# Optimization experiments

Hardware: AMD Instinct MI355X
Metric: run time of the kernel (lower is better)

The kernel has to match this reference:

```python
import jax, jax.numpy as jnp
import numpy as np

B, T, NB = 8, 120, 40
VD, WD = 2053, 300
H, E, NH, HD = 512, 256, 8, 64
SEG, NSEG = 12, 10
IDX = np.round(np.linspace(SEG - 1, T - 1, NSEG)).astype(int)  # segment endpoints


def setup_inputs():
    keys = iter(jax.random.split(jax.random.key(0), 64))
    def w(*shape):
        return jax.random.normal(next(keys), shape, jnp.float32) * 0.02
    z = lambda *s: jnp.zeros(s, jnp.float32)
    return dict(
        videos=jax.random.normal(next(keys), (B, T, NB, VD), jnp.float32),
        sub_glove=jax.random.normal(next(keys), (B, WD), jnp.float32),
        obj_glove=jax.random.normal(next(keys), (B, WD), jnp.float32),
        W_ev=w(VD - 5, E), b_ev=z(E),
        W_el=w(5, E), b_el=z(E),
        W_ew=w(WD, E), b_ew=z(E),
        W_sp1=w(2 * E, E), b_sp1=z(E), w_sp2=w(E),
        W_s2o=w(NB, E), b_s2o=z(E),
        W_o2s=w(NB, E), b_o2s=z(E),
        W_tv=w(H, H), b_tv=z(H),
        Wq=w(H, H), bq=z(H), Wk=w(H, H), bk=z(H), Wv=w(H, H), bv=z(H), Wo=w(H, H), bo=z(H),
        g1=jnp.ones(H, jnp.float32), be1=z(H),
        Wf1=w(H, H), bf1=z(H), Wf2=w(H, H), bf2=z(H),
        g2=jnp.ones(H, jnp.float32), be2=z(H),
        W_tr=w(H, H), b_tr=z(H),
        W_tb1=w(2 * H, H), b_tb1=z(H), w_tb2=w(H),
        W_ih=w(4 * H, H), W_hh=w(4 * H, H), b_ih=z(4 * H), b_hh=z(4 * H),
        W_l1=w(2 * H, H), b_l1=z(H), w_l2=w(H),
    )


def reference(videos, sub_glove, obj_glove, W_ev, b_ev, W_el, b_el, W_ew, b_ew,
              W_sp1, b_sp1, w_sp2, W_s2o, b_s2o, W_o2s, b_o2s, W_tv, b_tv,
              Wq, bq, Wk, bk, Wv, bv, Wo, bo, g1, be1, Wf1, bf1, Wf2, bf2, g2, be2,
              W_tr, b_tr, W_tb1, b_tb1, w_tb2, W_ih, W_hh, b_ih, b_hh, W_l1, b_l1, w_l2):
    relu = jax.nn.relu
    # spatialAtt (vectorized over batch; dropout = identity, eval mode)
    ve = relu(videos[..., :VD - 5] @ W_ev + b_ev) + relu(videos[..., VD - 5:] @ W_el + b_el)  # [B,T,NB,E]
    sub_e = relu(sub_glove @ W_ew + b_ew)  # [B,E]
    obj_e = relu(obj_glove @ W_ew + b_ew)

    def attend(word):  # additive attention over bboxes per frame
        wb = jnp.broadcast_to(word[:, None, None, :], ve.shape)
        s = jnp.tanh(jnp.concatenate([ve, wb], -1) @ W_sp1 + b_sp1) @ w_sp2  # [B,T,NB]
        a = jax.nn.softmax(s, -1)
        return jnp.einsum('btn,btne->bte', a, ve), a

    sub_feat, sub_att = attend(sub_e)
    obj_feat, obj_att = attend(obj_e)
    s2o = relu(sub_att @ W_s2o + b_s2o)  # msg_sub2obj on attention weights [B,T,NB]->[B,T,E]
    o2s = relu(obj_att @ W_o2s + b_o2s)
    ori_x = jnp.concatenate([sub_feat + o2s, obj_feat + s2o], -1)  # [B,T,H]
    rel = jnp.concatenate([sub_e, obj_e], -1)[:, None, :]  # [B,1,H]

    def ln(zz, g, b):
        m = zz.mean(-1, keepdims=True)
        v = jnp.mean((zz - m) ** 2, -1, keepdims=True)
        return (zz - m) * jax.lax.rsqrt(v + 1e-5) * g + b

    # transform_visual + 1-layer post-norm TransformerEncoder (relu FFN, dropout=identity)
    x = relu(ori_x @ W_tv + b_tv)
    q = (x @ Wq + bq).reshape(B, T, NH, HD)
    k = (x @ Wk + bk).reshape(B, T, NH, HD)
    v = (x @ Wv + bv).reshape(B, T, NH, HD)
    att = jax.nn.softmax(jnp.einsum('bqhd,bkhd->bhqk', q, k) / np.float32(np.sqrt(HD)), -1)
    ao = jnp.einsum('bhqk,bkhd->bqhd', att, v).reshape(B, T, H) @ Wo + bo
    x = ln(x + ao, g1, be1)
    x = ln(x + relu(x @ Wf1 + bf1) @ Wf2 + bf2, g2, be2)
    within = x  # [B,T,H]

    seg_in = within[:, IDX, :]  # [B,NSEG,H]
    tr = relu(rel @ W_tr + b_tr)
    ctx = jnp.broadcast_to(tr, seg_in.shape)
    beta2 = jax.nn.softmax(jnp.tanh(jnp.concatenate([seg_in, ctx], -1) @ W_tb1 + b_tb1) @ w_tb2, -1)  # [B,NSEG]

    # torch-convention LSTM (gates i,f,g,o); note attention weights are NOT applied to input (vfeat=input)
    def step(carry, xt):
        h, c = carry
        gates = xt @ W_ih.T + h @ W_hh.T + b_ih + b_hh
        i, f, g_, o = jnp.split(gates, 4, -1)
        c = jax.nn.sigmoid(f) * c + jax.nn.sigmoid(i) * jnp.tanh(g_)
        h = jax.nn.sigmoid(o) * jnp.tanh(c)
        return (h, c), h

    (hT, cT), _ = jax.lax.scan(step, (jnp.zeros((B, H), within.dtype), jnp.zeros((B, H), within.dtype)),
                               seg_in.transpose(1, 0, 2))

    ctx2 = jnp.broadcast_to(hT[:, None, :], within.shape)
    beta1 = jax.nn.softmax(jnp.tanh(jnp.concatenate([within, ctx2], -1) @ W_l1 + b_l1) @ w_l2, -1)  # [B,T]
    temp = beta1 + jnp.repeat(beta2, SEG, axis=1)  # temp[:,i] = beta1[:,i] + beta2[:,i//12]
    output = jnp.einsum('bt,bth->bh', temp, within)  # [B,H]
    return output, hT, cT, sub_att, obj_att, beta1, beta2
```

## Files before the change

### kernel.cpp

```cpp
#include <hip/hip_runtime.h>
#include <cstddef>
#include <cstdint>

#define B_ 8
#define T_ 120
#define NB_ 40
#define VD_ 2053
#define E_ 256
#define H_ 512
#define M_ 38400
#define R_ 960

static constexpr size_t OFF_VE    = 0;
static constexpr size_t OFF_SSUB  = OFF_VE + (size_t)M_ * E_;
static constexpr size_t OFF_SOBJ  = OFF_SSUB + M_;
static constexpr size_t OFF_WBS   = OFF_SOBJ + M_;
static constexpr size_t OFF_WBO   = OFF_WBS + B_ * E_;
static constexpr size_t OFF_TBIAS = OFF_WBO + B_ * E_;
static constexpr size_t OFF_ORIX  = OFF_TBIAS + B_ * H_;
static constexpr size_t OFF_X     = OFF_ORIX + (size_t)R_ * H_;
static constexpr size_t OFF_Q     = OFF_X    + (size_t)R_ * H_;
static constexpr size_t OFF_K     = OFF_Q    + (size_t)R_ * H_;
static constexpr size_t OFF_V     = OFF_K    + (size_t)R_ * H_;
static constexpr size_t OFF_AO    = OFF_V    + (size_t)R_ * H_;
// ... 156 lines not shown
      t[r][c] = src[(size_t)(kb * 64 + r) * 512 + nb * 64 + c];
    }
    __syncthreads();
#pragma unroll
    for (int i = 0; i < 16; ++i) {
      int idx = tid + 256 * i; int n = idx >> 6, kk = idx & 63;
      dst[(size_t)(nb * 64 + n) * 512 + kb * 64 + kk] = f2bf(t[kk][n]);
    }
  } else if (bid < 592) {
    int b2 = bid - 576;
    int kb = b2 >> 2, nb = b2 & 3;
#pragma unroll
    for (int i = 0; i < 16; ++i) {
      int idx = tid + 256 * i; int r = idx >> 6, c = idx & 63;
      t[r][c] = W_sp1[(size_t)(kb * 64 + r) * 256 + nb * 64 + c];
    }
    __syncthreads();
#pragma unroll
    for (int i = 0; i < 16; ++i) {
      int idx = tid + 256 * i; int n = idx >> 6, kk = idx & 63;
      wsp1bf[(size_t)(nb * 64 + n) * 256 + kb * 64 + kk] = f2bf(t[kk][n]);
    }
  } else if (bid < 656) {
    int b2 = bid - 592;
    int kb = b2 >> 3, nb = b2 & 7;
#pragma unroll
    for (int i = 0; i < 16; ++i) {
      int idx = tid + 256 * i; int r = idx >> 6, c = idx & 63;
      t[r][c] = W_l1[(size_t)(kb * 64 + r) * 512 + nb * 64 + c];
    }
    __syncthreads();
#pragma unroll
    for (int i = 0; i < 16; ++i) {
      int idx = tid + 256 * i; int n = idx >> 6, kk = idx & 63;
      wl1bf[(size_t)(nb * 64 + n) * 512 + kb * 64 + kk] = f2bf(t[kk][n]);
    }
  } else if (bid < 1680) {
    int i = (bid - 656) * 256 + tid;
    const float* s; unsigned short* d; int off;
    if (i < 131072) { s = W_ih; d = wihbf; off = i * 8; }
    else            { s = W_hh; d = whhbf; off = (i - 131072) * 8; }
    float f[8];
#pragma unroll
    for (int j = 0; j < 8; ++j) f[j] = s[off + j];
    *(short8*)(d + off) = mk8(f);
  } else if (bid == 1680) {
    for (int i = tid; i < 12288; i += 256) hz[i] = 0.f;
  } else {
    int b = bid - 1681;
    float* sg = shm;
    float* og = shm + 300;
    float* se = shm + 600;
    float* oe = shm + 856;
    float* trl = shm + 1112;
    for (int i = tid; i < 300; i += 256) { sg[i] = sub_g[b * 300 + i]; og[i] = obj_g[b * 300 + i]; }
    __syncthreads();
    {
      float a1 = b_ew[tid], a2 = a1;
      for (int w = 0; w < 300; ++w) {
        float we = W_ew[w * 256 + tid];
        a1 += sg[w] * we; a2 += og[w] * we;
      }
      se[tid] = fmaxf(a1, 0.f); oe[tid] = fmaxf(a2, 0.f);
    }
    __syncthreads();
    {
      float a1 = b_sp1[tid], a2 = a1;
      for (int e = 0; e < 256; ++e) {
        float ww = W_sp1[(256 + e) * 256 + tid];
        a1 += se[e] * ww; a2 += oe[e] * ww;
      }
      wbs[b * 256 + tid] = a1; wbo[b * 256 + tid] = a2;
    }
    for (int jj = 0; jj < 2; ++jj) {
      int j = tid + jj * 256;
      float a = b_tr[j];
      for (int i = 0; i < 256; ++i) a += se[i] * W_tr[i * 512 + j];
      for (int i = 0; i < 256; ++i) a += oe[i] * W_tr[(256 + i) * 512 + j];
      trl[j] = fmaxf(a, 0.f);
    }
    __syncthreads();
    for (int jj = 0; jj < 2; ++jj) {
      int j = tid + jj * 256;
      float a = b_tb1[j];
      for (int i = 0; i < 512; ++i) a += trl[i] * W_tb1[(size_t)(512 + i) * 512 + j];
      tbias[b * 512 + j] = a;
    }
  }
}

__global__ __launch_bounds__(256) void k_wconvT(const float* __restrict__ src,
                                                unsigned short* __restrict__ dst,
                                                int K, int N) {
  __shared__ float t[64][65];
  int nblk = N >> 6;
  int kb = blockIdx.x / nblk, nb = blockIdx.x - kb * nblk;
  int tid = threadIdx.x;
#pragma unroll
  for (int i = 0; i < 16; ++i) {
    int idx = tid + 256 * i;
    int r = idx >> 6, c = idx & 63;
    t[r][c] = src[(size_t)(kb * 64 + r) * N + nb * 64 + c];
  }
  __syncthreads();
#pragma unroll
  for (int i = 0; i < 16; ++i) {
    int idx = tid + 256 * i;
    int n = idx >> 6, kk = idx & 63;
    dst[(size_t)(nb * 64 + n) * K + kb * 64 + kk] = f2bf(t[kk][n]);
  }
}

__global__ __launch_bounds__(256) void k_wconv7(
    const float* __restrict__ w0, const float* __restrict__ w1,
    const float* __restrict__ w2, const float* __restrict__ w3,
    const float* __restrict__ w4, const float* __restrict__ w5,
    const float* __restrict__ w6, unsigned short* __restrict__ dstb) {
  __shared__ float t[64][65];
  int wsel = blockIdx.x >> 6, sub = blockIdx.x & 63;
  int kb = sub >> 3, nb = sub & 7;
  const float* src = wsel == 0 ? w0 : wsel == 1 ? w1 : wsel == 2 ? w2
                   : wsel == 3 ? w3 : wsel == 4 ? w4 : wsel == 5 ? w5 : w6;
  unsigned short* dst = dstb + (size_t)wsel * 262144;
  int tid = threadIdx.x;
#pragma unroll
  for (int i = 0; i < 16; ++i) {
    int idx = tid + 256 * i;
    int r = idx >> 6, c = idx & 63;
    t[r][c] = src[(size_t)(kb * 64 + r) * 512 + nb * 64 + c];
  }
  __syncthreads();
#pragma unroll
  for (int i = 0; i < 16; ++i) {
    int idx = tid + 256 * i;
    int n = idx >> 6, kk = idx & 63;
    dst[(size_t)(nb * 64 + n) * 512 + kb * 64 + kk] = f2bf(t[kk][n]);
  }
}

__global__ __launch_bounds__(256) void k_cvt2(const float* __restrict__ a,
                                              const float* __restrict__ b,
                                              unsigned short* __restrict__ da,
                                              unsigned short* __restrict__ db) {
  int i = blockIdx.x * 256 + threadIdx.x;
  const float* s; unsigned short* d; int off;
  if (i < 131072) { s = a; d = da; off = i * 8; }
  else            { s = b; d = db; off = (i - 131072) * 8; }
  float f[8];
#pragma unroll
  for (int j = 0; j < 8; ++j) f[j] = s[off + j];
  *(short8*)(d + off) = mk8(f);
}

__global__ __launch_bounds__(512) void k_gemm_ve_m97(
    const float* __restrict__ videos, const unsigned short* __restrict__ wtbf,
    const float* __restrict__ bev, const float* __restrict__ Wel,
    const float* __restrict__ bel, unsigned short* __restrict__ vebf) {
  __shared__ __align__(16) unsigned short lds[20480];
  int tid = threadIdx.x;
  int rowbase = blockIdx.x * 64;
  int lane = tid & 63, wid = tid >> 6;
  int l16 = lane & 15, lk = lane >> 4;

  int arow = tid >> 3, akc = tid & 7;
  const float* apA = videos + (size_t)(rowbase + arow) * VD_ + akc * 8;
  int dstA = arow * 64 + ((akc ^ (arow & 7)) * 8);
  const unsigned short* spB[4];
  int dstB[4];
#pragma unroll
  for (int i = 0; i < 4; ++i) {
    int g = tid + 512 * i;
    int n = g >> 3, kc = g & 7;
    spB[i] = wtbf + (size_t)n * 2048 + kc * 8;
    dstB[i] = 4096 + n * 64 + ((kc ^ (n & 7)) * 8);
  }
  float fa[8];
  short8 stB[4];
#pragma unroll
  for (int j = 0; j < 8; ++j) fa[j] = apA[j];
#pragma unroll
  for (int i = 0; i < 4; ++i) stB[i] = *(const short8*)(spB[i]);

  f32x4 acc[4][2] = {};
  for (int k0 = 0; k0 < 2048; k0 += 64) {
    short8 ha = mk8(fa);
    __syncthreads();
    *(short8*)(lds + dstA) = ha;
#pragma unroll
    for (int i = 0; i < 4; ++i) *(short8*)(lds + dstB[i]) = stB[i];
    __syncthreads();
    int kn = (k0 + 64 < 2048) ? k0 + 64 : 0;
#pragma unroll
    for (int j = 0; j < 8; ++j) fa[j] = apA[kn + j];
#pragma unroll
    for (int i = 0; i < 4; ++i) stB[i] = *(const short8*)(spB[i] + kn);
#pragma unroll
    for (int kk = 0; kk < 2; ++kk) {
      short8 a8[4], b8[2];
#pragma unroll
      for (int fm = 0; fm < 4; ++fm) {
        int row = fm * 16 + l16;
        a8[fm] = *(const short8*)(lds + row * 64 + (((kk * 4 + lk) ^ (row & 7)) * 8));
      }
#pragma unroll
      for (int fn = 0; fn < 2; ++fn) {
        int n = wid * 32 + fn * 16 + l16;
        b8[fn] = *(const short8*)(lds + 4096 + n * 64 + (((kk * 4 + lk) ^ (n & 7)) * 8));
      }
#pragma unroll
      for (int fm = 0; fm < 4; ++fm)
#pragma unroll
        for (int fn = 0; fn < 2; ++fn)
          acc[fm][fn] = __builtin_amdgcn_mfma_f32_16x16x32_bf16(
              a8[fm], b8[fn], acc[fm][fn], 0, 0, 0);
    }
  }
  float bevv[2], belv[2], w5[5][2];
#pragma unroll
  for (int fn = 0; fn < 2; ++fn) {
    int col = wid * 32 + fn * 16 + l16;
    bevv[fn] = bev[col]; belv[fn] = bel[col];
#pragma unroll
    for (int kk = 0; kk < 5; ++kk) w5[kk][fn] = Wel[kk * 256 + col];
  }
#pragma unroll
  for (int fm = 0; fm < 4; ++fm) {
#pragma unroll
    for (int r = 0; r < 4; ++r) {
      int grow = rowbase + fm * 16 + lk * 4 + r;
      const float* vt = videos + (size_t)grow * VD_ + 2048;
      float t0 = vt[0], t1 = vt[1], t2 = vt[2], t3 = vt[3], t4 = vt[4];
      unsigned short* vob = vebf + (size_t)grow * 256;
#pragma unroll
      for (int fn = 0; fn < 2; ++fn) {
        int col = wid * 32 + fn * 16 + l16;
        float s2 = belv[fn] + t0 * w5[0][fn] + t1 * w5[1][fn] + t2 * w5[2][fn] +
                   t3 * w5[3][fn] + t4 * w5[4][fn];
        float vvv = fmaxf(acc[fm][fn][r] + bevv[fn], 0.f) + fmaxf(s2, 0.f);
        vob[col] = f2bf(vvv);
      }
    }
  }
}

__global__ __launch_bounds__(256) void k_score_bf(
    const unsigned short* __restrict__ vebf, const unsigned short* __restrict__ wsp1,
    const float* __restrict__ w_sp2, const float* __restrict__ wbs,
    const float* __restrict__ wbo, float* __restrict__ s_sub,
    float* __restrict__ s_obj) {
  __shared__ float reds[4][64], redo_[4][64];
  int tid = threadIdx.x;
  int rowbase = blockIdx.x * 64;
  int lane = tid & 63, wid = tid >> 6;
  int l16 = lane & 15, lk = lane >> 4;
  const unsigned short* ap[4];
  const unsigned short* bp[4];
#pragma unroll
  for (int fm = 0; fm < 4; ++fm)
    ap[fm] = vebf + (size_t)(rowbase + fm * 16 + l16) * 256 + lk * 8;
#pragma unroll
  for (int fn = 0; fn < 4; ++fn)
    bp[fn] = wsp1 + (size_t)(wid * 64 + fn * 16 + l16) * 256 + lk * 8;
  f32x4 acc[4][4] = {};
#pragma unroll 2
  for (int k0 = 0; k0 < 256; k0 += 32) {
    short8 a8[4], b8[4];
#pragma unroll
    for (int fm = 0; fm < 4; ++fm) a8[fm] = *(const short8*)(ap[fm] + k0);
#pragma unroll
    for (int fn = 0; fn < 4; ++fn) b8[fn] = *(const short8*)(bp[fn] + k0);
#pragma unroll
    for (int fm = 0; fm < 4; ++fm)
#pragma unroll
      for (int fn = 0; fn < 4; ++fn)
        acc[fm][fn] = __builtin_amdgcn_mfma_f32_16x16x32_bf16(
            a8[fm], b8[fn], acc[fm][fn], 0, 0, 0);
  }
  int b = rowbase / 4800;
  float w2[4], bs[4], bo[4];
#pragma unroll
  for (int fn = 0; fn < 4; ++fn) {
    int col = wid * 64 + fn * 16 + l16;
    w2[fn] = w_sp2[col];
    bs[fn] = wbs[b * 256 + col];
    bo[fn] = wbo[b * 256 + col];
  }
  float ps[4][4], po[4][4];
#pragma unroll
  for (int fm = 0; fm < 4; ++fm)
#pragma unroll
    for (int r = 0; r < 4; ++r) {
      float aps = 0, apo = 0;
#pragma unroll
      for (int fn = 0; fn < 4; ++fn) {
        float t = acc[fm][fn][r];
        aps += fast_tanh(t + bs[fn]) * w2[fn];
        apo += fast_tanh(t + bo[fn]) * w2[fn];
      }
      ps[fm][r] = aps;
      po[fm][r] = apo;
    }
#pragma unroll
  for (int m = 1; m < 16; m <<= 1) {
#pragma unroll
    for (int fm = 0; fm < 4; ++fm)
#pragma unroll
      for (int r = 0; r < 4; ++r) {
        ps[fm][r] += __shfl_xor(ps[fm][r], m);
        po[fm][r] += __shfl_xor(po[fm][r], m);
      }
  }
  if (l16 == 0) {
#pragma unroll
    for (int fm = 0; fm < 4; ++fm)
#pragma unroll
      for (int r = 0; r < 4; ++r) {
        int row = fm * 16 + lk * 4 + r;
        reds[wid][row] = ps[fm][r];
        redo_[wid][row] = po[fm][r];
      }
  }
  __syncthreads();
  if (tid < 64) {
    float s1 = reds[0][tid] + reds[1][tid] + reds[2][tid] + reds[3][tid];
    float s2 = redo_[0][tid] + redo_[1][tid] + redo_[2][tid] + redo_[3][tid];
    s_sub[rowbase + tid] = s1;
    s_obj[rowbase + tid] = s2;
  }
}

__global__ __launch_bounds__(256) void k_attend_bf(
    const float* __restrict__ s_sub, const float* __restrict__ s_obj,
    const unsigned short* __restrict__ vebf, const float* __restrict__ W_s2o,
    const float* __restrict__ b_s2o, const float* __restrict__ W_o2s,
    const float* __restrict__ b_o2s, float* __restrict__ out_satt,
    float* __restrict__ out_oatt, float* __restrict__ orix) {
  int row = blockIdx.x;
  int tid = threadIdx.x;
  __shared__ float alds[2][40];
  int wv = tid >> 6, lane = tid & 63;
  if (wv < 2) {
    const float* sarr = (wv ? s_obj : s_sub) + row * 40;
    float v = (lane < 40) ? sarr[lane] : -1e30f;
    float mx = wredmax(v);
    float e = (lane < 40) ? __expf(v - mx) : 0.f;
    float sm = wredsum(e);
    float p = e / sm;
    if (lane < 40) {
      alds[wv][lane] = p;
      (wv ? out_oatt : out_satt)[row * 40 + lane] = p;
    }
  }
  __syncthreads();
  int e = tid;
  const unsigned short* vrow = vebf + (size_t)row * 40 * 256;
  float sf = 0, of = 0, s2o = b_s2o[e], o2s = b_o2s[e];
  for (int n = 0; n < 40; ++n) {
    float as = alds[0][n], aob = alds[1][n];
    float vv = bf2f(vrow[n * 256 + e]);
    sf += as * vv;
    of += aob * vv;
    s2o += as * W_s2o[n * 256 + e];
    o2s += aob * W_o2s[n * 256 + e];
  }
  s2o = fmaxf(s2o, 0.f);
  o2s = fmaxf(o2s, 0.f);
  orix[(size_t)row * 512 + e] = sf + o2s;
  orix[(size_t)row * 512 + 256 + e] = of + s2o;
// ... 19 lines not shown
  for (int k0 = 0; k0 < 2048; k0 += 64) {
#pragma unroll
    for (int kk = 0; kk < 2; ++kk) {
      int ko = k0 + kk * 32;
      short8 a8[4], b8[4];
#pragma unroll
      for (int fm = 0; fm < 4; ++fm) {
        const float* a = ap[fm] + ko;
        float f[8];
#pragma unroll
        for (int j = 0; j < 8; ++j) f[j] = a[j];
        a8[fm] = mk8(f);
      }
#pragma unroll
      for (int fn = 0; fn < 4; ++fn) b8[fn] = *(const short8*)(bp[fn] + ko);
#pragma unroll
      for (int fm = 0; fm < 4; ++fm)
#pragma unroll
        for (int fn = 0; fn < 4; ++fn)
          acc[fm][fn] = __builtin_amdgcn_mfma_f32_16x16x32_bf16(
              a8[fm], b8[fn], acc[fm][fn], 0, 0, 0);
    }
    if ((k0 & 255) == 192) __builtin_amdgcn_s_barrier();
  }
  float bevv[4], belv[4], w5[5][4];
#pragma unroll
  for (int fn = 0; fn < 4; ++fn) {
    int col = wid * 64 + fn * 16 + l16;
    bevv[fn] = bev[col]; belv[fn] = bel[col];
#pragma unroll
    for (int kk = 0; kk < 5; ++kk) w5[kk][fn] = Wel[kk * 256 + col];
  }
#pragma unroll
  for (int fm = 0; fm < 4; ++fm) {
#pragma unroll
    for (int r = 0; r < 4; ++r) {
      int grow = rowbase + fm * 16 + lk * 4 + r;
      const float* vt = videos + (size_t)grow * VD_ + 2048;
      float t0 = vt[0], t1 = vt[1], t2 = vt[2], t3 = vt[3], t4 = vt[4];
      float* vo = ve + (size_t)grow * 256;
#pragma unroll
      for (int fn = 0; fn < 4; ++fn) {
        int col = wid * 64 + fn * 16 + l16;
        float s2 = belv[fn] + t0 * w5[0][fn] + t1 * w5[1][fn] + t2 * w5[2][fn] +
                   t3 * w5[3][fn] + t4 * w5[4][fn];
        vo[col] = fmaxf(acc[fm][fn][r] + bevv[fn], 0.f) + fmaxf(s2, 0.f);
      }
    }
  }
}

__global__ __launch_bounds__(256) void k_score(
    const float* __restrict__ ve, const float* __restrict__ W_sp1,
    const float* __restrict__ w_sp2, const float* __restrict__ wbs,
    const float* __restrict__ wbo, float* __restrict__ s_sub,
    float* __restrict__ s_obj) {
  __shared__ float vel[32][264];
  int tid = threadIdx.x;
  int rowbase = blockIdx.x * 32;
  for (int i = tid; i < 2048; i += 256) {
    int r = i >> 6, c = (i & 63) << 2;
    *(float4*)&vel[r][c] = *(const float4*)&ve[(size_t)(rowbase + r) * 256 + c];
  }
  __syncthreads();
  int wv = tid >> 6, lane = tid & 63;
  int r0 = wv * 8;
  float acc[8][4] = {};
  for (int k = 0; k < 256; ++k) {
    float w4[4];
#pragma unroll
    for (int c = 0; c < 4; ++c) w4[c] = W_sp1[(size_t)k * 256 + c * 64 + lane];
#pragma unroll
    for (int m = 0; m < 8; ++m) {
      float a = vel[r0 + m][k];
#pragma unroll
      for (int c = 0; c < 4; ++c) acc[m][c] += a * w4[c];
    }
  }
  int b = rowbase / 4800;
  float w2[4], bs[4], bo[4];
#pragma unroll
  for (int c = 0; c < 4; ++c) {
    int col = c * 64 + lane;
    w2[c] = w_sp2[col];
    bs[c] = wbs[b * 256 + col];
    bo[c] = wbo[b * 256 + col];
  }
#pragma unroll
  for (int m = 0; m < 8; ++m) {
    float ps = 0, po = 0;
#pragma unroll
    for (int c = 0; c < 4; ++c) {
      float t = acc[m][c];
      ps += fast_tanh(t + bs[c]) * w2[c];
      po += fast_tanh(t + bo[c]) * w2[c];
    }
    ps = wredsum(ps);
    po = wredsum(po);
    if (lane == 0) {
      s_sub[rowbase + r0 + m] = ps;
      s_obj[rowbase + r0 + m] = po;
    }
  }
}

__global__ __launch_bounds__(256) void k_attend(
    const float* __restrict__ s_sub, const float* __restrict__ s_obj,
    const float* __restrict__ ve, const float* __restrict__ W_s2o,
    const float* __restrict__ b_s2o, const float* __restrict__ W_o2s,
    const float* __restrict__ b_o2s, float* __restrict__ out_satt,
    float* __restrict__ out_oatt, float* __restrict__ orix) {
  int row = blockIdx.x;
  int tid = threadIdx.x;
  __shared__ float alds[2][40];
  int wv = tid >> 6, lane = tid & 63;
  if (wv < 2) {
    const float* sarr = (wv ? s_obj : s_sub) + row * 40;
    float v = (lane < 40) ? sarr[lane] : -1e30f;
    float mx = wredmax(v);
    float e = (lane < 40) ? __expf(v - mx) : 0.f;
    float sm = wredsum(e);
    float p = e / sm;
    if (lane < 40) {
      alds[wv][lane] = p;
      (wv ? out_oatt : out_satt)[row * 40 + lane] = p;
    }
  }
  __syncthreads();
  int e = tid;
  const float* vrow = ve + (size_t)row * 40 * 256;
  float sf = 0, of = 0, s2o = b_s2o[e], o2s = b_o2s[e];
  for (int n = 0; n < 40; ++n) {
    float as = alds[0][n], aob = alds[1][n];
    float vv = vrow[n * 256 + e];
    sf += as * vv;
    of += aob * vv;
    s2o += as * W_s2o[n * 256 + e];
    o2s += aob * W_o2s[n * 256 + e];
  }
  s2o = fmaxf(s2o, 0.f);
  o2s = fmaxf(o2s, 0.f);
  orix[(size_t)row * 512 + e] = sf + o2s;
  orix[(size_t)row * 512 + 256 + e] = of + s2o;
}

__global__ __launch_bounds__(256) void k_gemm_h(
    const float* __restrict__ A, const unsigned short* __restrict__ WT,
    const float* __restrict__ b0, const float* __restrict__ b1,
    const float* __restrict__ b2, float* __restrict__ Cbase, int ntiles,
    int relu) {
  int tid = threadIdx.x;
  int bid = blockIdx.x;
  int mt = bid / ntiles, nt = bid - mt * ntiles;
  int rowbase = mt * 64;
  int lane = tid & 63, wid = tid >> 6;
  int wrow = wid >> 1, wcol = wid & 1;
  int l16 = lane & 15, lk = lane >> 4;
  const float* ap[2];
  const unsigned short* bp[2];
#pragma unroll
  for (int fm = 0; fm < 2; ++fm)
    ap[fm] = A + (size_t)(rowbase + wrow * 32 + fm * 16 + l16) * 512 + lk * 8;
#pragma unroll
  for (int fn = 0; fn < 2; ++fn)
    bp[fn] = WT + (size_t)(nt * 64 + wcol * 32 + fn * 16 + l16) * 512 + lk * 8;
  f32x4 acc[2][2] = {};
  for (int k0 = 0; k0 < 512; k0 += 64) {
#pragma unroll
    for (int kk = 0; kk < 2; ++kk) {
      int ko = k0 + kk * 32;
      short8 a8[2], b8[2];
#pragma unroll
      for (int fm = 0; fm < 2; ++fm) {
        float4 x = *(const float4*)(ap[fm] + ko);
        float4 y = *(const float4*)(ap[fm] + ko + 4);
        float f[8] = {x.x, x.y, x.z, x.w, y.x, y.y, y.z, y.w};
        a8[fm] = mk8(f);
      }
#pragma unroll
      for (int fn = 0; fn < 2; ++fn) b8[fn] = *(const short8*)(bp[fn] + ko);
#pragma unroll
      for (int fm = 0; fm < 2; ++fm)
#pragma unroll
        for (int fn = 0; fn < 2; ++fn)
          acc[fm][fn] = __builtin_amdgcn_mfma_f32_16x16x32_bf16(
              a8[fm], b8[fn], acc[fm][fn], 0, 0, 0);
    }
  }
#pragma unroll
  for (int fn = 0; fn < 2; ++fn) {
    int cg = nt * 64 + wcol * 32 + fn * 16 + l16;
    int third = cg >> 9, c = cg & 511;
    const float* bb = third == 0 ? b0 : (third == 1 ? b1 : b2);
    float bv = bb[c];
    float* outp = Cbase + (size_t)third * ((size_t)R_ * H_);
#pragma unroll
    for (int fm = 0; fm < 2; ++fm) {
#pragma unroll
      for (int r = 0; r < 4; ++r) {
        int grow = rowbase + wrow * 32 + fm * 16 + lk * 4 + r;
        float v = acc[fm][fn][r] + bv;
        if (relu) v = fmaxf(v, 0.f);
        outp[(size_t)grow * 512 + c] = v;
      }
    }
  }
}

__global__ __launch_bounds__(256) void k_xb(
    const float* __restrict__ win, const unsigned short* __restrict__ wih,
    const float* __restrict__ b_ih, const float* __restrict__ b_hh,
    float* __restrict__ gx, const float* __restrict__ W_tb1,
    const float* __restrict__ w_tb2, const float* __restrict__ tbias,
    float* __restrict__ z2) {
  __shared__ float xr[512];
  __shared__ float red[256];
  int bid0 = blockIdx.x;
  int tid = threadIdx.x;
  if (bid0 < 64) {
    int bid = bid0;
    int mt = bid >> 5, nt = bid & 31;
    int lane = tid & 63, wid = tid >> 6;
    int wrow = wid >> 1, wcol = wid & 1;
    int l16 = lane & 15, lk = lane >> 4;
    const float* ap[2];
    bool av[2];
#pragma unroll
    for (int fm = 0; fm < 2; ++fm) {
      int base = mt * 64 + wrow * 32 + fm * 16;
      av[fm] = base < 80;
      int grow = base + l16;
      int s = grow >> 3, b = grow & 7;
      ap[fm] = av[fm] ? (win + (size_t)(b * 120 + 11 + 12 * s) * 512 + lk * 8)
                      : win;
    }
    const unsigned short* bp[2];
#pragma unroll
    for (int fn = 0; fn < 2; ++fn)
      bp[fn] = wih + (size_t)(nt * 64 + wcol * 32 + fn * 16 + l16) * 512 + lk * 8;
    f32x4 acc[2][2] = {};
    for (int k0 = 0; k0 < 512; k0 += 64) {
#pragma unroll
      for (int kk = 0; kk < 2; ++kk) {
        int ko = k0 + kk * 32;
        short8 a8[2], b8[2];
#pragma unroll
        for (int fm = 0; fm < 2; ++fm) {
          if (av[fm]) {
            float4 x = *(const float4*)(ap[fm] + ko);
            float4 y = *(const float4*)(ap[fm] + ko + 4);
            float f[8] = {x.x, x.y, x.z, x.w, y.x, y.y, y.z, y.w};
            a8[fm] = mk8(f);
          } else {
            a8[fm] = short8{0, 0, 0, 0, 0, 0, 0, 0};
          }
        }
#pragma unroll
        for (int fn = 0; fn < 2; ++fn) b8[fn] = *(const short8*)(bp[fn] + ko);
#pragma unroll
        for (int fm = 0; fm < 2; ++fm)
#pragma unroll
          for (int fn = 0; fn < 2; ++fn)
            acc[fm][fn] = __builtin_amdgcn_mfma_f32_16x16x32_bf16(
                a8[fm], b8[fn], acc[fm][fn], 0, 0, 0);
      }
    }
#pragma unroll
    for (int fn = 0; fn < 2; ++fn) {
      int cg = nt * 64 + wcol * 32 + fn * 16 + l16;
      float bv = b_ih[cg] + b_hh[cg];
#pragma unroll
      for (int fm = 0; fm < 2; ++fm) {
        if (!av[fm]) continue;
#pragma unroll
        for (int r = 0; r < 4; ++r) {
          int grow = mt * 64 + wrow * 32 + fm * 16 + lk * 4 + r;
          if (grow < 80) gx[(size_t)grow * 2048 + cg] = acc[fm][fn][r] + bv;
        }
      }
    }
  } else {
    int bid = bid0 - 64;
    int b = bid / 10, si = bid - b * 10;
    int trow = b * 120 + 11 + 12 * si;
    for (int i = tid; i < 512; i += 256) xr[i] = win[(size_t)trow * 512 + i];
    __syncthreads();
    float val = 0;
    for (int jj = 0; jj < 2; ++jj) {
      int j = tid + jj * 256;
      float a = tbias[b * 512 + j];
      for (int i = 0; i < 512; ++i) a += xr[i] * W_tb1[(size_t)i * 512 + j];
      val += fast_tanh(a) * w_tb2[j];
    }
    red[tid] = val;
    __syncthreads();
    for (int s = 128; s; s >>= 1) {
      if (tid < s) red[tid] += red[tid + s];
      __syncthreads();
    }
    if (tid == 0) z2[bid] = red[0];
  }
}

__global__ __launch_bounds__(256) void k_xproj(
    const float* __restrict__ win, const unsigned short* __restrict__ wih,
    const float* __restrict__ b_ih, const float* __restrict__ b_hh,
    float* __restrict__ gx) {
  int bid = blockIdx.x;
  int mt = bid >> 5, nt = bid & 31;
  int tid = threadIdx.x;
  int lane = tid & 63, wid = tid >> 6;
  int wrow = wid >> 1, wcol = wid & 1;
  int l16 = lane & 15, lk = lane >> 4;
  const float* ap[2];
  bool av[2];
#pragma unroll
  for (int fm = 0; fm < 2; ++fm) {
    int base = mt * 64 + wrow * 32 + fm * 16;
    av[fm] = base < 80;
    int grow = base + l16;
    int s = grow >> 3, b = grow & 7;
    ap[fm] = av[fm] ? (win + (size_t)(b * 120 + 11 + 12 * s) * 512 + lk * 8)
                    : win;
  }
  const unsigned short* bp[2];
#pragma unroll
  for (int fn = 0; fn < 2; ++fn)
    bp[fn] = wih + (size_t)(nt * 64 + wcol * 32 + fn * 16 + l16) * 512 + lk * 8;
  f32x4 acc[2][2] = {};
  for (int k0 = 0; k0 < 512; k0 += 64) {
#pragma unroll
    for (int kk = 0; kk < 2; ++kk) {
      int ko = k0 + kk * 32;
      short8 a8[2], b8[2];
#pragma unroll
      for (int fm = 0; fm < 2; ++fm) {
        if (av[fm]) {
          float4 x = *(const float4*)(ap[fm] + ko);
          float4 y = *(const float4*)(ap[fm] + ko + 4);
          float f[8] = {x.x, x.y, x.z, x.w, y.x, y.y, y.z, y.w};
          a8[fm] = mk8(f);
        } else {
          a8[fm] = short8{0, 0, 0, 0, 0, 0, 0, 0};
        }
      }
#pragma unroll
      for (int fn = 0; fn < 2; ++fn) b8[fn] = *(const short8*)(bp[fn] + ko);
#pragma unroll
      for (int fm = 0; fm < 2; ++fm)
#pragma unroll
        for (int fn = 0; fn < 2; ++fn)
          acc[fm][fn] = __builtin_amdgcn_mfma_f32_16x16x32_bf16(
              a8[fm], b8[fn], acc[fm][fn], 0, 0, 0);
    }
  }
#pragma unroll
  for (int fn = 0; fn < 2; ++fn) {
// ... 294 lines not shown
    const float* __restrict__ l1, const float* __restrict__ z2,
    const float* __restrict__ within, const float* __restrict__ hT,
    const float* __restrict__ cT, float* __restrict__ dout) {
  int b = blockIdx.x;
  int tid = threadIdx.x;
  __shared__ float temp[120];
  __shared__ float b2[10];
  int wv = tid >> 6, lane = tid & 63;
  if (wv == 1) {
    float v = (lane < 10) ? z2[b * 10 + lane] : -1e30f;
    float mx = wredmax(v);
    float e = (lane < 10) ? __expf(v - mx) : 0.f;
    float sm = wredsum(e);
    if (lane < 10) {
      float p = e / sm;
      b2[lane] = p;
      dout[O_B2 + b * 10 + lane] = p;
    }
  }
  if (wv == 0) {
    float v1 = l1[b * 120 + lane];
    float v2 = (lane + 64 < 120) ? l1[b * 120 + 64 + lane] : -1e30f;
    float mx = wredmax(fmaxf(v1, v2));
    float e1 = __expf(v1 - mx);
    float e2 = (lane + 64 < 120) ? __expf(v2 - mx) : 0.f;
    float sm = wredsum(e1 + e2);
    float p1 = e1 / sm;
    dout[O_B1 + b * 120 + lane] = p1;
    temp[lane] = p1;
    if (lane + 64 < 120) {
      float p2 = e2 / sm;
      dout[O_B1 + b * 120 + 64 + lane] = p2;
      temp[64 + lane] = p2;
    }
  }
  __syncthreads();
  for (int t = tid; t < 120; t += 256) temp[t] += b2[t / 12];
  __syncthreads();
  for (int hh = tid; hh < 512; hh += 256) {
    float o = 0;
    for (int t = 0; t < 120; ++t) o += temp[t] * within[(size_t)(b * 120 + t) * 512 + hh];
    dout[O_OUT + b * 512 + hh] = o;
    dout[O_HT + b * 512 + hh] = hT[b * 512 + hh];
    dout[O_CT + b * 512 + hh] = cT[b * 512 + hh];
  }
}

extern "C" void kernel_launch(void* const* d_in, const int* in_sizes, int n_in,
                              void* d_out, int out_size, void* d_ws, size_t ws_size,
                              hipStream_t stream) {
  const float* videos = (const float*)d_in[0];
  const float* sub_g  = (const float*)d_in[1];
  const float* obj_g  = (const float*)d_in[2];
  const float* W_ev   = (const float*)d_in[3];
  const float* b_ev   = (const float*)d_in[4];
  const float* W_el   = (const float*)d_in[5];
  const float* b_el   = (const float*)d_in[6];
  const float* W_ew   = (const float*)d_in[7];
  const float* b_ew   = (const float*)d_in[8];
  const float* W_sp1  = (const float*)d_in[9];
  const float* b_sp1  = (const float*)d_in[10];
  const float* w_sp2  = (const float*)d_in[11];
  const float* W_s2o  = (const float*)d_in[12];
  const float* b_s2o  = (const float*)d_in[13];
  const float* W_o2s  = (const float*)d_in[14];
  const float* b_o2s  = (const float*)d_in[15];
  const float* W_tv   = (const float*)d_in[16];
  const float* b_tv   = (const float*)d_in[17];
  const float* Wq     = (const float*)d_in[18];
  const float* bq     = (const float*)d_in[19];
  const float* Wk     = (const float*)d_in[20];
  const float* bk     = (const float*)d_in[21];
  const float* Wv     = (const float*)d_in[22];
  const float* bv     = (const float*)d_in[23];
  const float* Wo     = (const float*)d_in[24];
  const float* bo     = (const float*)d_in[25];
  const float* g1     = (const float*)d_in[26];
  const float* be1    = (const float*)d_in[27];
  const float* Wf1    = (const float*)d_in[28];
  const float* bf1    = (const float*)d_in[29];
  const float* Wf2    = (const float*)d_in[30];
  const float* bf2    = (const float*)d_in[31];
  const float* g2     = (const float*)d_in[32];
  const float* be2    = (const float*)d_in[33];
  const float* W_tr   = (const float*)d_in[34];
  const float* b_tr   = (const float*)d_in[35];
  const float* W_tb1  = (const float*)d_in[36];
  const float* b_tb1  = (const float*)d_in[37];
  const float* w_tb2  = (const float*)d_in[38];
  const float* W_ih   = (const float*)d_in[39];
  const float* W_hh   = (const float*)d_in[40];
  const float* b_ih   = (const float*)d_in[41];
  const float* b_hh   = (const float*)d_in[42];
  const float* W_l1   = (const float*)d_in[43];
  const float* b_l1   = (const float*)d_in[44];
  const float* w_l2   = (const float*)d_in[45];

  float* out = (float*)d_out;
  float* w = (float*)d_ws;

  float* ve_p   = w + OFF_VE;
  float* ssub_p = w + OFF_SSUB;
  float* sobj_p = w + OFF_SOBJ;
  float* wbs_p  = w + OFF_WBS;
  float* wbo_p  = w + OFF_WBO;
  float* tb_p   = w + OFF_TBIAS;
  float* orix_p = w + OFF_ORIX;
  float* x_p    = w + OFF_X;
  float* q_p    = w + OFF_Q;
  float* k_p    = w + OFF_K;
  float* v_p    = w + OFF_V;
  float* ao_p   = w + OFF_AO;
  float* attn_p = w + OFF_ATTN;
  float* x1_p   = w + OFF_X1;
  float* f1_p   = w + OFF_F1;
  float* f2_p   = w + OFF_F2;
  float* win_p  = w + OFF_WIN;
  float* z2_p   = w + OFF_Z2;
  float* h_p    = w + OFF_H0;
  float* c_p    = h_p + 2 * 4096;
  float* hb_p   = w + OFF_HB;
  float* l1_p   = w + OFF_L1;

  unsigned short* wtbase = (unsigned short*)(w + OFF_WT);
  unsigned short* wevbf = wtbase;
  unsigned short* w7bf  = wtbase + 524288;
  unsigned short* wtvbf = w7bf;
  unsigned short* wqbf  = w7bf + 1 * 262144;
  unsigned short* wobf  = w7bf + 4 * 262144;
  unsigned short* wf1bf = w7bf + 5 * 262144;
  unsigned short* wf2bf = w7bf + 6 * 262144;
  unsigned short* wsp1bf = w7bf + 7 * 262144;
  unsigned short* wihbf  = (unsigned short*)(w + OFF_WIH);
  unsigned short* whhbf  = (unsigned short*)(w + OFF_WHH);
  unsigned short* wl1bf  = (unsigned short*)(w + OFF_WL1B);
  unsigned short* winbf_p = (unsigned short*)(w + OFF_WINBF);
  unsigned short* vebf_p = (unsigned short*)(w + OFF_VEBF);
  float* gx_p = w + OFF_Q;
  const bool big = ws_size >= (size_t)OFF_END * 4;

  if (big) {
    k_wprep<<<1689, 256, 0, stream>>>(W_ev, W_tv, Wq, Wk, Wv, Wo, Wf1, Wf2,
                                      W_sp1, W_l1, W_ih, W_hh, sub_g, obj_g,
                                      W_ew, b_ew, b_sp1, W_tr, b_tr, W_tb1,
                                      b_tb1, wevbf, w7bf, wsp1bf, wl1bf, wihbf,
                                      whhbf, h_p, wbs_p, wbo_p, tb_p);
    k_gemm_ve_m97<<<600, 512, 0, stream>>>(videos, wevbf, b_ev, W_el, b_el,
                                           vebf_p);
    k_score_bf<<<600, 256, 0, stream>>>(vebf_p, wsp1bf, w_sp2, wbs_p, wbo_p,
                                        ssub_p, sobj_p);
    k_attend_bf<<<960, 256, 0, stream>>>(ssub_p, sobj_p, vebf_p, W_s2o, b_s2o,
                                         W_o2s, b_o2s, out + O_SATT,
                                         out + O_OATT, orix_p);
    k_gemm_h<<<120, 256, 0, stream>>>(orix_p, wtvbf, b_tv, b_tv, b_tv, x_p, 8, 1);
    k_gemm_h<<<360, 256, 0, stream>>>(x_p, wqbf, bq, bk, bv, q_p, 24, 0);
    k_mha<<<256, 256, 0, stream>>>(q_p, k_p, v_p, ao_p);
    k_gemm_h<<<120, 256, 0, stream>>>(ao_p, wobf, bo, bo, bo, attn_p, 8, 0);
    k_ln<<<240, 256, 0, stream>>>(x_p, attn_p, g1, be1, x1_p, nullptr);
    k_gemm_h<<<120, 256, 0, stream>>>(x1_p, wf1bf, bf1, bf1, bf1, f1_p, 8, 1);
    k_gemm_h<<<120, 256, 0, stream>>>(f1_p, wf2bf, bf2, bf2, bf2, f2_p, 8, 0);
    k_ln<<<240, 256, 0, stream>>>(x1_p, f2_p, g2, be2, win_p, winbf_p);
    k_xb<<<144, 256, 0, stream>>>(win_p, wihbf, b_ih, b_hh, gx_p, W_tb1, w_tb2,
                                  tb_p, z2_p);
    for (int s = 0; s < 10; ++s) {
      float* hin = h_p + (s & 1) * 4096;
      float* hout = h_p + ((s & 1) ^ 1) * 4096;
      k_lstm_step<<<32, 128, 0, stream>>>(hin, whhbf, gx_p, s, hout, c_p);
    }
    k_hbias<<<16, 256, 0, stream>>>(h_p, W_l1, b_l1, hb_p);
    k_beta1_bf<<<15, 256, 0, stream>>>(winbf_p, wl1bf, w_l2, hb_p, l1_p);
    k_final<<<8, 256, 0, stream>>>(l1_p, z2_p, win_p, h_p, c_p, out);
  } else {
    unsigned short* wihbf_a = (unsigned short*)(w + OFF_Q + 163840);
    unsigned short* whhbf_a = (unsigned short*)(w + OFF_Q + 688128);
    k_zero<<<48, 256, 0, stream>>>(h_p, 3 * 4096);
    k_small0<<<8, 256, 0, stream>>>(sub_g, obj_g, W_ew, b_ew, W_sp1, b_sp1,
                                    W_tr, b_tr, W_tb1, b_tb1, wbs_p, wbo_p, tb_p);
    k_wconvT<<<128, 256, 0, stream>>>(W_ev, wevbf, 2048, 256);
    k_wconv7<<<448, 256, 0, stream>>>(W_tv, Wq, Wk, Wv, Wo, Wf1, Wf2, w7bf);
    k_gemm_ve_mfma<<<600, 256, 0, stream>>>(videos, wevbf, b_ev, W_el, b_el, ve_p);
    k_score<<<1200, 256, 0, stream>>>(ve_p, W_sp1, w_sp2, wbs_p, wbo_p, ssub_p, sobj_p);
    k_attend<<<960, 256, 0, stream>>>(ssub_p, sobj_p, ve_p, W_s2o, b_s2o, W_o2s,
                                      b_o2s, out + O_SATT, out + O_OATT, orix_p);
    k_gemm_h<<<120, 256, 0, stream>>>(orix_p, wtvbf, b_tv, b_tv, b_tv, x_p, 8, 1);
    k_gemm_h<<<360, 256, 0, stream>>>(x_p, wqbf, bq, bk, bv, q_p, 24, 0);
    k_mha<<<256, 256, 0, stream>>>(q_p, k_p, v_p, ao_p);
    k_gemm_h<<<120, 256, 0, stream>>>(ao_p, wobf, bo, bo, bo, attn_p, 8, 0);
    k_ln<<<240, 256, 0, stream>>>(x_p, attn_p, g1, be1, x1_p, nullptr);
    k_gemm_h<<<120, 256, 0, stream>>>(x1_p, wf1bf, bf1, bf1, bf1, f1_p, 8, 1);
    k_gemm_h<<<120, 256, 0, stream>>>(f1_p, wf2bf, bf2, bf2, bf2, f2_p, 8, 0);
    k_ln<<<240, 256, 0, stream>>>(x1_p, f2_p, g2, be2, win_p, nullptr);
    k_cvt2<<<1024, 256, 0, stream>>>(W_ih, W_hh, wihbf_a, whhbf_a);
    k_xproj<<<64, 256, 0, stream>>>(win_p, wihbf_a, b_ih, b_hh, gx_p);
    k_beta2<<<80, 256, 0, stream>>>(win_p, W_tb1, w_tb2, tb_p, z2_p);
    for (int s = 0; s < 10; ++s) {
      float* hin = h_p + (s & 1) * 4096;
      float* hout = h_p + ((s & 1) ^ 1) * 4096;
      k_lstm_step<<<32, 128, 0, stream>>>(hin, whhbf_a, gx_p, s, hout, c_p);
    }
    k_hbias<<<16, 256, 0, stream>>>(h_p, W_l1, b_l1, hb_p);
    k_beta1<<<240, 256, 0, stream>>>(win_p, W_l1, w_l2, hb_p, l1_p);
    k_final<<<8, 256, 0, stream>>>(l1_p, z2_p, win_p, h_p, c_p, out);
  }
}
```

Before: 633.6 us.

## Double-buffer A prefetch in video GEMM and halve row tile of hidden GEMMs

The large video-embedding GEMM now keeps two register buffers of A data and unrolls the K loop by two, so global loads for A run two steps ahead of use and hide more memory latency. The hidden-size GEMM kernel moves from a 64-row to a 32-row tile, with each wave doing one 16-row fragment, and the grid doubles to match. This gives more blocks for 960-row problems on a large GPU, at the cost of more B-weight reloads and more register use in the video GEMM.

```diff
diff --git a/kernel.cpp b/kernel.cpp
--- a/kernel.cpp
+++ b/kernel.cpp
@@ -332,6 +332,42 @@
   *(short8*)(d + off) = mk8(f);
 }
 
+#define VESTEP(FA, KA, KB)                                                 \
+  {                                                                        \
+    short8 ha = mk8(FA);                                                   \
+    __syncthreads();                                                       \
+    *(short8*)(lds + dstA) = ha;                                           \
+    _Pragma("unroll")                                                      \
+    for (int i = 0; i < 4; ++i) *(short8*)(lds + dstB[i]) = stB[i];        \
+    __syncthreads();                                                       \
+    _Pragma("unroll")                                                      \
+    for (int j = 0; j < 8; ++j) FA[j] = apA[(KA) + j];                     \
+    _Pragma("unroll")                                                      \
+    for (int i = 0; i < 4; ++i) stB[i] = *(const short8*)(spB[i] + (KB));  \
+    _Pragma("unroll")                                                      \
+    for (int kk = 0; kk < 2; ++kk) {                                       \
+      short8 a8[4], b8[2];                                                 \
+      _Pragma("unroll")                                                    \
+      for (int fm = 0; fm < 4; ++fm) {                                     \
+        int row = fm * 16 + l16;                                           \
+        a8[fm] = *(const short8*)(lds + row * 64 +                         \
+                                  (((kk * 4 + lk) ^ (row & 7)) * 8));      \
+      }                                                                    \
+      _Pragma("unroll")                                                    \
+      for (int fn = 0; fn < 2; ++fn) {                                     \
+        int n = wid * 32 + fn * 16 + l16;                                  \
+        b8[fn] = *(const short8*)(lds + 4096 + n * 64 +                    \
+                                  (((kk * 4 + lk) ^ (n & 7)) * 8));        \
+      }                                                                    \
+      _Pragma("unroll")                                                    \
+      for (int fm = 0; fm < 4; ++fm)                                       \
+        _Pragma("unroll")                                                  \
+        for (int fn = 0; fn < 2; ++fn)                                     \
+          acc[fm][fn] = __builtin_amdgcn_mfma_f32_16x16x32_bf16(           \
+              a8[fm], b8[fn], acc[fm][fn], 0, 0, 0);                       \
+    }                                                                      \
+  }
+
 __global__ __launch_bounds__(512) void k_gemm_ve_m97(
     const float* __restrict__ videos, const unsigned short* __restrict__ wtbf,
     const float* __restrict__ bev, const float* __restrict__ Wel,
@@ -354,46 +390,23 @@
     spB[i] = wtbf + (size_t)n * 2048 + kc * 8;
     dstB[i] = 4096 + n * 64 + ((kc ^ (n & 7)) * 8);
   }
-  float fa[8];
+  float fa0[8], fa1[8];
   short8 stB[4];
 #pragma unroll
-  for (int j = 0; j < 8; ++j) fa[j] = apA[j];
+  for (int j = 0; j < 8; ++j) fa0[j] = apA[j];
 #pragma unroll
   for (int i = 0; i < 4; ++i) stB[i] = *(const short8*)(spB[i]);
+#pragma unroll
+  for (int j = 0; j < 8; ++j) fa1[j] = apA[64 + j];
 
   f32x4 acc[4][2] = {};
-  for (int k0 = 0; k0 < 2048; k0 += 64) {
-    short8 ha = mk8(fa);
-    __syncthreads();
-    *(short8*)(lds + dstA) = ha;
-#pragma unroll
-    for (int i = 0; i < 4; ++i) *(short8*)(lds + dstB[i]) = stB[i];
-    __syncthreads();
-    int kn = (k0 + 64 < 2048) ? k0 + 64 : 0;
-#pragma unroll
-    for (int j = 0; j < 8; ++j) fa[j] = apA[kn + j];
-#pragma unroll
-    for (int i = 0; i < 4; ++i) stB[i] = *(const short8*)(spB[i] + kn);
-#pragma unroll
-    for (int kk = 0; kk < 2; ++kk) {
-      short8 a8[4], b8[2];
-#pragma unroll
-      for (int fm = 0; fm < 4; ++fm) {
-        int row = fm * 16 + l16;
-        a8[fm] = *(const short8*)(lds + row * 64 + (((kk * 4 + lk) ^ (row & 7)) * 8));
-      }
-#pragma unroll
-      for (int fn = 0; fn < 2; ++fn) {
-        int n = wid * 32 + fn * 16 + l16;
-        b8[fn] = *(const short8*)(lds + 4096 + n * 64 + (((kk * 4 + lk) ^ (n & 7)) * 8));
-      }
-#pragma unroll
-      for (int fm = 0; fm < 4; ++fm)
-#pragma unroll
-        for (int fn = 0; fn < 2; ++fn)
-          acc[fm][fn] = __builtin_amdgcn_mfma_f32_16x16x32_bf16(
-              a8[fm], b8[fn], acc[fm][fn], 0, 0, 0);
-    }
+  for (int k0 = 0; k0 < 2048; k0 += 128) {
+    int ka0 = k0 + 128; if (ka0 >= 2048) ka0 -= 2048;
+    int kb0 = k0 + 64;
+    VESTEP(fa0, ka0, kb0);
+    int ka1 = k0 + 192; if (ka1 >= 2048) ka1 -= 2048;
+    int kb1 = k0 + 128; if (kb1 >= 2048) kb1 -= 2048;
+    VESTEP(fa1, ka1, kb1);
   }
   float bevv[2], belv[2], w5[5][2];
 #pragma unroll
@@ -719,39 +732,29 @@
   int tid = threadIdx.x;
   int bid = blockIdx.x;
   int mt = bid / ntiles, nt = bid - mt * ntiles;
-  int rowbase = mt * 64;
+  int rowbase = mt * 32;
   int lane = tid & 63, wid = tid >> 6;
   int wrow = wid >> 1, wcol = wid & 1;
   int l16 = lane & 15, lk = lane >> 4;
-  const float* ap[2];
+  const float* ap = A + (size_t)(rowbase + wrow * 16 + l16) * 512 + lk * 8;
   const unsigned short* bp[2];
-#pragma unroll
-  for (int fm = 0; fm < 2; ++fm)
-    ap[fm] = A + (size_t)(rowbase + wrow * 32 + fm * 16 + l16) * 512 + lk * 8;
 #pragma unroll
   for (int fn = 0; fn < 2; ++fn)
     bp[fn] = WT + (size_t)(nt * 64 + wcol * 32 + fn * 16 + l16) * 512 + lk * 8;
-  f32x4 acc[2][2] = {};
+  f32x4 acc[2] = {};
   for (int k0 = 0; k0 < 512; k0 += 64) {
 #pragma unroll
     for (int kk = 0; kk < 2; ++kk) {
       int ko = k0 + kk * 32;
-      short8 a8[2], b8[2];
-#pragma unroll
-      for (int fm = 0; fm < 2; ++fm) {
-        float4 x = *(const float4*)(ap[fm] + ko);
-        float4 y = *(const float4*)(ap[fm] + ko + 4);
-        float f[8] = {x.x, x.y, x.z, x.w, y.x, y.y, y.z, y.w};
-        a8[fm] = mk8(f);
+      float4 x = *(const float4*)(ap + ko);
+      float4 y = *(const float4*)(ap + ko + 4);
+      float f[8] = {x.x, x.y, x.z, x.w, y.x, y.y, y.z, y.w};
+      short8 a8 = mk8(f);
+#pragma unroll
+      for (int fn = 0; fn < 2; ++fn) {
+        short8 b8 = *(const short8*)(bp[fn] + ko);
+        acc[fn] = __builtin_amdgcn_mfma_f32_16x16x32_bf16(a8, b8, acc[fn], 0, 0, 0);
       }
-#pragma unroll
-      for (int fn = 0; fn < 2; ++fn) b8[fn] = *(const short8*)(bp[fn] + ko);
-#pragma unroll
-      for (int fm = 0; fm < 2; ++fm)
-#pragma unroll
-        for (int fn = 0; fn < 2; ++fn)
-          acc[fm][fn] = __builtin_amdgcn_mfma_f32_16x16x32_bf16(
-              a8[fm], b8[fn], acc[fm][fn], 0, 0, 0);
     }
   }
 #pragma unroll
@@ -762,14 +765,11 @@
     float bv = bb[c];
     float* outp = Cbase + (size_t)third * ((size_t)R_ * H_);
 #pragma unroll
-    for (int fm = 0; fm < 2; ++fm) {
-#pragma unroll
-      for (int r = 0; r < 4; ++r) {
-        int grow = rowbase + wrow * 32 + fm * 16 + lk * 4 + r;
-        float v = acc[fm][fn][r] + bv;
-        if (relu) v = fmaxf(v, 0.f);
-        outp[(size_t)grow * 512 + c] = v;
-      }
+    for (int r = 0; r < 4; ++r) {
+      int grow = rowbase + wrow * 16 + lk * 4 + r;
+      float v = acc[fn][r] + bv;
+      if (relu) v = fmaxf(v, 0.f);
+      outp[(size_t)grow * 512 + c] = v;
     }
   }
 }
@@ -1370,13 +1370,13 @@
     k_attend_bf<<<960, 256, 0, stream>>>(ssub_p, sobj_p, vebf_p, W_s2o, b_s2o,
                                          W_o2s, b_o2s, out + O_SATT,
                                          out + O_OATT, orix_p);
-    k_gemm_h<<<120, 256, 0, stream>>>(orix_p, wtvbf, b_tv, b_tv, b_tv, x_p, 8, 1);
-    k_gemm_h<<<360, 256, 0, stream>>>(x_p, wqbf, bq, bk, bv, q_p, 24, 0);
+    k_gemm_h<<<240, 256, 0, stream>>>(orix_p, wtvbf, b_tv, b_tv, b_tv, x_p, 8, 1);
+    k_gemm_h<<<720, 256, 0, stream>>>(x_p, wqbf, bq, bk, bv, q_p, 24, 0);
     k_mha<<<256, 256, 0, stream>>>(q_p, k_p, v_p, ao_p);
-    k_gemm_h<<<120, 256, 0, stream>>>(ao_p, wobf, bo, bo, bo, attn_p, 8, 0);
+    k_gemm_h<<<240, 256, 0, stream>>>(ao_p, wobf, bo, bo, bo, attn_p, 8, 0);
     k_ln<<<240, 256, 0, stream>>>(x_p, attn_p, g1, be1, x1_p, nullptr);
-    k_gemm_h<<<120, 256, 0, stream>>>(x1_p, wf1bf, bf1, bf1, bf1, f1_p, 8, 1);
-    k_gemm_h<<<120, 256, 0, stream>>>(f1_p, wf2bf, bf2, bf2, bf2, f2_p, 8, 0);
+    k_gemm_h<<<240, 256, 0, stream>>>(x1_p, wf1bf, bf1, bf1, bf1, f1_p, 8, 1);
+    k_gemm_h<<<240, 256, 0, stream>>>(f1_p, wf2bf, bf2, bf2, bf2, f2_p, 8, 0);
     k_ln<<<240, 256, 0, stream>>>(x1_p, f2_p, g2, be2, win_p, winbf_p);
     k_xb<<<144, 256, 0, stream>>>(win_p, wihbf, b_ih, b_hh, gx_p, W_tb1, w_tb2,
                                   tb_p, z2_p);
@@ -1400,13 +1400,13 @@
     k_score<<<1200, 256, 0, stream>>>(ve_p, W_sp1, w_sp2, wbs_p, wbo_p, ssub_p, sobj_p);
     k_attend<<<960, 256, 0, stream>>>(ssub_p, sobj_p, ve_p, W_s2o, b_s2o, W_o2s,
                                       b_o2s, out + O_SATT, out + O_OATT, orix_p);
-    k_gemm_h<<<120, 256, 0, stream>>>(orix_p, wtvbf, b_tv, b_tv, b_tv, x_p, 8, 1);
-    k_gemm_h<<<360, 256, 0, stream>>>(x_p, wqbf, bq, bk, bv, q_p, 24, 0);
+    k_gemm_h<<<240, 256, 0, stream>>>(orix_p, wtvbf, b_tv, b_tv, b_tv, x_p, 8, 1);
+    k_gemm_h<<<720, 256, 0, stream>>>(x_p, wqbf, bq, bk, bv, q_p, 24, 0);
     k_mha<<<256, 256, 0, stream>>>(q_p, k_p, v_p, ao_p);
-    k_gemm_h<<<120, 256, 0, stream>>>(ao_p, wobf, bo, bo, bo, attn_p, 8, 0);
+    k_gemm_h<<<240, 256, 0, stream>>>(ao_p, wobf, bo, bo, bo, attn_p, 8, 0);
     k_ln<<<240, 256, 0, stream>>>(x_p, attn_p, g1, be1, x1_p, nullptr);
-    k_gemm_h<<<120, 256, 0, stream>>>(x1_p, wf1bf, bf1, bf1, bf1, f1_p, 8, 1);
-    k_gemm_h<<<120, 256, 0, stream>>>(f1_p, wf2bf, bf2, bf2, bf2, f2_p, 8, 0);
+    k_gemm_h<<<240, 256, 0, stream>>>(x1_p, wf1bf, bf1, bf1, bf1, f1_p, 8, 1);
+    k_gemm_h<<<240, 256, 0, stream>>>(f1_p, wf2bf, bf2, bf2, bf2, f2_p, 8, 0);
     k_ln<<<240, 256, 0, stream>>>(x1_p, f2_p, g2, be2, win_p, nullptr);
     k_cvt2<<<1024, 256, 0, stream>>>(W_ih, W_hh, wihbf_a, whhbf_a);
     k_xproj<<<64, 256, 0, stream>>>(win_p, wihbf_a, b_ih, b_hh, gx_p);
```

Result: no change. 631.0 us (-0.4%).
